# Optimization experiments

Measured on AMD Instinct MI355X. Metric: run time of the kernel, lower is better.

Reference implementation:

```python
import jax, jax.numpy as jnp
import numpy as np

B, C = 4096, 16384
SCALE = 16.0
MARGIN = 0.1
NEG_INF = -10000.0
HARD_SCALE = 1.0 + 0.012
HARD_SHIFT = 0.012


def setup_inputs() -> dict:
    key = jax.random.key(0)
    k1, k2, k3 = jax.random.split(key, 3)
    inputs = jax.random.normal(k1, (B, C), dtype=jnp.float32)
    targets = jax.random.randint(k2, (B,), 0, C, dtype=jnp.int64)
    # camera-positive mask: 0/1 floats
    pos_cam_mask = jax.random.bernoulli(k3, 0.5, (B, C)).astype(jnp.float32)
    mask = jnp.zeros((B, C), dtype=bool)  # unused by the module (overwritten)
    return {"inputs": inputs, "targets": targets, "mask": mask, "pos_cam_mask": pos_cam_mask}


def reference(inputs, targets, mask, pos_cam_mask):
    b, c = inputs.shape
    rows = jnp.arange(b)
    one_hot = jax.nn.one_hot(targets, c, dtype=inputs.dtype)  # (B, C)
    # camera-masked logits; non-positive-cam entries pushed to -10000
    cam_inputs = pos_cam_mask * inputs + (1.0 - pos_cam_mask) * NEG_INF
    gt = inputs[rows, targets]  # (B,) target logit, pre-modification
    hard_mask = cam_inputs >= gt[:, None]  # (B, C)
    # rescale hard examples: x <- 1.012 * x + 0.012 where hard
    x = jnp.where(hard_mask, HARD_SCALE * inputs + HARD_SHIFT, inputs)
    # restore original gt logit at target positions (scatter_)
    x = jnp.where(one_hot > 0, gt[:, None], x)
    output = SCALE * (x - one_hot * MARGIN)
    # mean cross-entropy
    logp = jax.nn.log_softmax(output, axis=-1)
    loss = -jnp.mean(logp[rows, targets])
    return loss
```

## Files before the change

### kernel.cpp

```cpp
#include <hip/hip_runtime.h>


#define B_ 4096
#define C_ 16384
#define LOG2E 1.44269504088896340736f

template <bool USE_ATOMIC>
__global__ __launch_bounds__(256, 3) void coscam_loss_kernel(
    const float* __restrict__ inputs,
    const int*   __restrict__ targets,
    const float* __restrict__ pos_mask,
    float*       __restrict__ sink)
{
    const int row = blockIdx.x;
    const int tid = threadIdx.x;

    const float* __restrict__ rin = inputs   + (size_t)row * C_;
    const float* __restrict__ rpm = pos_mask + (size_t)row * C_;

    const int   t     = targets[row];
    const float gt    = rin[t];
    const float pos_t = rpm[t];

    const float wt      = gt - 0.1f;
    const float out_t   = 16.0f * wt;
    const float shift   = fmaxf(out_t, 40.0f);
    const float nshift2 = -shift * LOG2E;
    const float k16l2e  = 16.0f * LOG2E;

    float4 xs[16], ps[16];
    #pragma unroll
    for (int u = 0; u < 16; ++u) {
        const int c = u * 1024 + tid * 4;
        xs[u] = *(const float4*)(rin + c);
        ps[u] = *(const float4*)(rpm + c);
    }

    float acc0 = 0.0f, acc1 = 0.0f, acc2 = 0.0f, acc3 = 0.0f;
    #pragma unroll
    for (int u = 0; u < 16; ++u) {
        const float4 x4 = xs[u];
        const float4 p4 = ps[u];
        const float w0 = ((p4.x > 0.5f) && (x4.x >= gt)) ? fmaf(1.012f, x4.x, 0.012f) : x4.x;
        const float w1 = ((p4.y > 0.5f) && (x4.y >= gt)) ? fmaf(1.012f, x4.y, 0.012f) : x4.y;
        const float w2 = ((p4.z > 0.5f) && (x4.z >= gt)) ? fmaf(1.012f, x4.z, 0.012f) : x4.z;
        const float w3 = ((p4.w > 0.5f) && (x4.w >= gt)) ? fmaf(1.012f, x4.w, 0.012f) : x4.w;
        acc0 += __builtin_amdgcn_exp2f(fmaf(w0, k16l2e, nshift2));
        acc1 += __builtin_amdgcn_exp2f(fmaf(w1, k16l2e, nshift2));
        acc2 += __builtin_amdgcn_exp2f(fmaf(w2, k16l2e, nshift2));
        acc3 += __builtin_amdgcn_exp2f(fmaf(w3, k16l2e, nshift2));
    }

    float s = (acc0 + acc1) + (acc2 + acc3);

    #pragma unroll
    for (int off = 32; off > 0; off >>= 1)
        s += __shfl_down(s, off);

    __shared__ float red_s[4];
    const int wave = tid >> 6;
    const int lane = tid & 63;
    if (lane == 0) red_s[wave] = s;
    __syncthreads();

    if (tid == 0) {
        float total = (red_s[0] + red_s[1]) + (red_s[2] + red_s[3]);
        const float w_wrong = (pos_t > 0.5f) ? fmaf(1.012f, gt, 0.012f) : gt;
        total += __builtin_amdgcn_exp2f(fmaf(wt,      k16l2e, nshift2))
               - __builtin_amdgcn_exp2f(fmaf(w_wrong, k16l2e, nshift2));
        const float loss_row = (__logf(total) + shift) - out_t;
        if (USE_ATOMIC) {
            atomicAdd(sink, loss_row * (1.0f / (float)B_));
        } else {
            sink[row] = loss_row;
        }
    }
}

__global__ __launch_bounds__(256, 1) void coscam_reduce_kernel(
    const float* __restrict__ partial,
    float*       __restrict__ out)
{
    const int tid = threadIdx.x;
    float s = 0.0f;
    #pragma unroll
    for (int u = 0; u < 16; ++u)
        s += partial[u * 256 + tid];

    #pragma unroll
    for (int off = 32; off > 0; off >>= 1)
        s += __shfl_down(s, off);

    __shared__ float red_s[4];
    if ((tid & 63) == 0) red_s[tid >> 6] = s;
    __syncthreads();

    if (tid == 0) {
        float total = (red_s[0] + red_s[1]) + (red_s[2] + red_s[3]);
        out[0] = total * (1.0f / (float)B_);
    }
}

extern "C" void kernel_launch(void* const* d_in, const int* in_sizes, int n_in,
                              void* d_out, int out_size, void* d_ws, size_t ws_size,
                              hipStream_t stream) {
    const float* inputs   = (const float*)d_in[0];
    const int*   targets  = (const int*)  d_in[1];
    const float* pos_mask = (const float*)d_in[3];
    float* out = (float*)d_out;

    if (d_ws != nullptr && ws_size >= (size_t)B_ * sizeof(float)) {
        float* partial = (float*)d_ws;
        coscam_loss_kernel<false><<<dim3(B_), dim3(256), 0, stream>>>(
            inputs, targets, pos_mask, partial);
        coscam_reduce_kernel<<<dim3(1), dim3(256), 0, stream>>>(partial, out);
    } else {
        (void)hipMemsetAsync(out, 0, sizeof(float), stream);
        coscam_loss_kernel<true><<<dim3(B_), dim3(256), 0, stream>>>(
            inputs, targets, pos_mask, out);
    }
}
```

Measured before the change: 596.0 us.

## Split each row across four blocks with partial sums and final log reduction

Each row is now processed by four blocks, each covering a quarter of the columns, which write partial exp sums. The block that owns the target column applies the target-logit correction and saves gt. A single reduce kernel then combines the four partials per row, takes the log and averages. The point is smaller blocks with fewer registers, so occupancy rises (launch bounds 8) and latency hiding for this memory-bound read improves, at the cost of redundant gt loads per block and a slightly heavier reduce.

```diff
diff --git a/kernel.cpp b/kernel.cpp
--- a/kernel.cpp
+++ b/kernel.cpp
@@ -5,12 +5,116 @@
 #define C_ 16384
 #define LOG2E 1.44269504088896340736f
 
-template <bool USE_ATOMIC>
-__global__ __launch_bounds__(256, 3) void coscam_loss_kernel(
+__global__ __launch_bounds__(256, 8) void coscam_partial_kernel(
     const float* __restrict__ inputs,
     const int*   __restrict__ targets,
     const float* __restrict__ pos_mask,
-    float*       __restrict__ sink)
+    float*       __restrict__ partial,
+    float*       __restrict__ gt_ws)
+{
+    const int part = blockIdx.x & 3;
+    const int row  = blockIdx.x >> 2;
+    const int tid  = threadIdx.x;
+
+    const float* __restrict__ rin = inputs   + (size_t)row * C_;
+    const float* __restrict__ rpm = pos_mask + (size_t)row * C_;
+
+    const int   t     = targets[row];
+    const float gt    = rin[t];
+    const float pos_t = rpm[t];
+
+    const float wt      = gt - 0.1f;
+    const float out_t   = 16.0f * wt;
+    const float shift   = fmaxf(out_t, 40.0f);
+    const float nshift2 = -shift * LOG2E;
+    const float k16l2e  = 16.0f * LOG2E;
+
+    const int cbase = part * 4096 + tid * 4;
+    float4 xs[4], ps[4];
+    #pragma unroll
+    for (int u = 0; u < 4; ++u) {
+        const int c = cbase + u * 1024;
+        xs[u] = *(const float4*)(rin + c);
+        ps[u] = *(const float4*)(rpm + c);
+    }
+
+    float acc0 = 0.0f, acc1 = 0.0f, acc2 = 0.0f, acc3 = 0.0f;
+    #pragma unroll
+    for (int u = 0; u < 4; ++u) {
+        const float4 x4 = xs[u];
+        const float4 p4 = ps[u];
+        const float w0 = ((p4.x > 0.5f) && (x4.x >= gt)) ? fmaf(1.012f, x4.x, 0.012f) : x4.x;
+        const float w1 = ((p4.y > 0.5f) && (x4.y >= gt)) ? fmaf(1.012f, x4.y, 0.012f) : x4.y;
+        const float w2 = ((p4.z > 0.5f) && (x4.z >= gt)) ? fmaf(1.012f, x4.z, 0.012f) : x4.z;
+        const float w3 = ((p4.w > 0.5f) && (x4.w >= gt)) ? fmaf(1.012f, x4.w, 0.012f) : x4.w;
+        acc0 += __builtin_amdgcn_exp2f(fmaf(w0, k16l2e, nshift2));
+        acc1 += __builtin_amdgcn_exp2f(fmaf(w1, k16l2e, nshift2));
+        acc2 += __builtin_amdgcn_exp2f(fmaf(w2, k16l2e, nshift2));
+        acc3 += __builtin_amdgcn_exp2f(fmaf(w3, k16l2e, nshift2));
+    }
+
+    float s = (acc0 + acc1) + (acc2 + acc3);
+
+    #pragma unroll
+    for (int off = 32; off > 0; off >>= 1)
+        s += __shfl_down(s, off);
+
+    __shared__ float red_s[4];
+    const int wave = tid >> 6;
+    const int lane = tid & 63;
+    if (lane == 0) red_s[wave] = s;
+    __syncthreads();
+
+    if (tid == 0) {
+        float total = (red_s[0] + red_s[1]) + (red_s[2] + red_s[3]);
+        if (part == (t >> 12)) {
+            const float w_wrong = (pos_t > 0.5f) ? fmaf(1.012f, gt, 0.012f) : gt;
+            total += __builtin_amdgcn_exp2f(fmaf(wt,      k16l2e, nshift2))
+                   - __builtin_amdgcn_exp2f(fmaf(w_wrong, k16l2e, nshift2));
+            gt_ws[row] = gt;
+        }
+        partial[blockIdx.x] = total;
+    }
+}
+
+__global__ __launch_bounds__(256, 1) void coscam_reduce_kernel(
+    const float* __restrict__ partial,
+    const float* __restrict__ gt_ws,
+    float*       __restrict__ out)
+{
+    const int tid = threadIdx.x;
+    float acc = 0.0f;
+    #pragma unroll
+    for (int u = 0; u < 16; ++u) {
+        const int r = u * 256 + tid;
+        const float4 p4 = *(const float4*)(partial + r * 4);
+        const float gt  = gt_ws[r];
+        const float wt    = gt - 0.1f;
+        const float out_t = 16.0f * wt;
+        const float shift = fmaxf(out_t, 40.0f);
+        const float total = (p4.x + p4.y) + (p4.z + p4.w);
+        acc += (__logf(total) + shift) - out_t;
+    }
+
+    #pragma unroll
+    for (int off = 32; off > 0; off >>= 1)
+        acc += __shfl_down(acc, off);
+
+    __shared__ float red_s[4];
+    if ((tid & 63) == 0) red_s[tid >> 6] = acc;
+    __syncthreads();
+
+    if (tid == 0) {
+        float total = (red_s[0] + red_s[1]) + (red_s[2] + red_s[3]);
+        out[0] = total * (1.0f / (float)B_);
+    }
+}
+
+__global__ __launch_bounds__(256, 3) void coscam_loss_atomic_kernel(
+    const float* __restrict__ inputs,
+    const int*   __restrict__ targets,
+    const float* __restrict__ pos_mask,
+    float*       __restrict__ out)
 {
     const int row = blockIdx.x;
     const int tid = threadIdx.x;
@@ -69,35 +173,7 @@
         total += __builtin_amdgcn_exp2f(fmaf(wt,      k16l2e, nshift2))
                - __builtin_amdgcn_exp2f(fmaf(w_wrong, k16l2e, nshift2));
         const float loss_row = (__logf(total) + shift) - out_t;
-        if (USE_ATOMIC) {
-            atomicAdd(sink, loss_row * (1.0f / (float)B_));
-        } else {
-            sink[row] = loss_row;
-        }
-    }
-}
-
-__global__ __launch_bounds__(256, 1) void coscam_reduce_kernel(
-    const float* __restrict__ partial,
-    float*       __restrict__ out)
-{
-    const int tid = threadIdx.x;
-    float s = 0.0f;
-    #pragma unroll
-    for (int u = 0; u < 16; ++u)
-        s += partial[u * 256 + tid];
-
-    #pragma unroll
-    for (int off = 32; off > 0; off >>= 1)
-        s += __shfl_down(s, off);
-
-    __shared__ float red_s[4];
-    if ((tid & 63) == 0) red_s[tid >> 6] = s;
-    __syncthreads();
-
-    if (tid == 0) {
-        float total = (red_s[0] + red_s[1]) + (red_s[2] + red_s[3]);
-        out[0] = total * (1.0f / (float)B_);
+        atomicAdd(out, loss_row * (1.0f / (float)B_));
     }
 }
 
@@ -109,14 +185,16 @@
     const float* pos_mask = (const float*)d_in[3];
     float* out = (float*)d_out;
 
-    if (d_ws != nullptr && ws_size >= (size_t)B_ * sizeof(float)) {
+    const size_t ws_need = (size_t)(B_ * 4 + B_) * sizeof(float);
+    if (d_ws != nullptr && ws_size >= ws_need) {
         float* partial = (float*)d_ws;
-        coscam_loss_kernel<false><<<dim3(B_), dim3(256), 0, stream>>>(
-            inputs, targets, pos_mask, partial);
-        coscam_reduce_kernel<<<dim3(1), dim3(256), 0, stream>>>(partial, out);
+        float* gt_ws   = partial + B_ * 4;
+        coscam_partial_kernel<<<dim3(B_ * 4), dim3(256), 0, stream>>>(
+            inputs, targets, pos_mask, partial, gt_ws);
+        coscam_reduce_kernel<<<dim3(1), dim3(256), 0, stream>>>(partial, gt_ws, out);
     } else {
         (void)hipMemsetAsync(out, 0, sizeof(float), stream);
-        coscam_loss_kernel<true><<<dim3(B_), dim3(256), 0, stream>>>(
+        coscam_loss_atomic_kernel<<<dim3(B_), dim3(256), 0, stream>>>(
             inputs, targets, pos_mask, out);
     }
 }
```

After: 600.0 us. About the same (+0.7%).
